# Optimization experiments

Measured on AMD Instinct MI355X. Metric: run time of the kernel, lower is better.

## Reference

```python
import jax, jax.numpy as jnp
import numpy as np
import math

N, E, C, H = 16384, 8192, 256, 8
NNZ = 262144  # incidence pairs, avg vertex degree 16


def setup_inputs() -> dict:
    key = jax.random.key(0)
    ks = jax.random.split(key, 12)
    s = 1.0 / math.sqrt(C)
    inp = {
        "X": jax.random.normal(ks[0], (N, C), dtype=jnp.float32),
        "v_ids": jax.random.randint(ks[1], (NNZ,), 0, N, dtype=jnp.int32),
        "e_ids": jax.random.randint(ks[2], (NNZ,), 0, E, dtype=jnp.int32),
        # Linear params stored as [in, out]; y = x @ W + b  (matches torch x @ W.T + b)
        "Wq": jax.random.uniform(ks[3], (C, C), jnp.float32, -s, s),
        "bq": jax.random.uniform(ks[4], (C,), jnp.float32, -s, s),
        "Wk": jax.random.uniform(ks[5], (C, C), jnp.float32, -s, s),
        "bk": jax.random.uniform(ks[6], (C,), jnp.float32, -s, s),
        "Wv": jax.random.uniform(ks[7], (C, C), jnp.float32, -s, s),
        "bv": jax.random.uniform(ks[8], (C,), jnp.float32, -s, s),
        "Wke": jax.random.uniform(ks[9], (C, C), jnp.float32, -s, s),
        "bke": jax.random.uniform(ks[10], (C,), jnp.float32, -s, s),
    }
    return inp


def reference(X, v_ids, e_ids, Wq, bq, Wk, bk, Wv, bv, Wke, bke):
    d = C // H
    scale = 1.0 / math.sqrt(d)

    Q = (X @ Wq + bq).reshape(N, H, d)
    K = (X @ Wk + bk).reshape(N, H, d)
    V = (X @ Wv + bv).reshape(N, H, d)

    # hg.v2e_aggregation(X, 'mean'): segment-mean of incident vertex features per hyperedge
    sums = jax.ops.segment_sum(X[v_ids], e_ids, num_segments=E)          # [E, C]
    cnt = jax.ops.segment_sum(jnp.ones((NNZ,), X.dtype), e_ids, num_segments=E)
    Xe = sums / jnp.maximum(cnt, 1.0)[:, None]                            # [E, C]

    Ke = Xe @ Wke + bke                                                   # [E, C]
    Qe = X @ Wq + bq                                                      # [N, C]

    # per-node attention over heads: [N, H, H]
    attn_n = jax.nn.softmax(jnp.einsum('nhd,ngd->nhg', Q, K) * scale, axis=-1)
    X_node = jnp.einsum('nhg,ngd->nhd', attn_n, V).reshape(N, C)          # [N, C]

    # node -> hyperedge attention: [N, E]
    attn_e = jax.nn.softmax((Qe @ Ke.T) * scale, axis=-1)
    X_hyperedge = attn_e @ Xe                                             # [N, C]

    out = X_node + X_hyperedge
    # is_last=False: ReLU; bn=None; dropout in eval mode (identity)
    return jax.nn.relu(out)
```

## Files before the change

### kernel.cpp

```cpp
#include <hip/hip_runtime.h>

typedef unsigned short u16;
typedef unsigned int u32;
typedef __attribute__((ext_vector_type(4))) float f32x4;
typedef __attribute__((ext_vector_type(16))) float f32x16;
typedef __attribute__((ext_vector_type(8))) short bf16x8;
typedef __attribute__((ext_vector_type(4))) short bf16x4;
typedef __attribute__((ext_vector_type(4))) u16 u16x4;

#define N_NODES 16384
#define N_EDGES 8192
#define FK_SCALE 0.17677669529663687f
#define LOG2E 1.4426950408889634f
#define C1EXP (FK_SCALE * LOG2E)

typedef const u32 __attribute__((address_space(1))) gu32;
typedef u32 __attribute__((address_space(3))) lu32;

__device__ __forceinline__ void gl_lds16(const void* g, void* l) {
  __builtin_amdgcn_global_load_lds((gu32*)g, (lu32*)l, 16, 0, 0);
}

__device__ __forceinline__ float b2f(u16 u) {
  return __builtin_bit_cast(float, (u32)u << 16);
}
__device__ __forceinline__ u16 f2b(float f) {
  u32 u = __builtin_bit_cast(u32, f);
  u += 0x7fffu + ((u >> 16) & 1u);
  return (u16)(u >> 16);
}

__global__ __launch_bounds__(256) void k_prep(const float* __restrict__ X,
                                              const int* __restrict__ e_ids,
                                              u16* __restrict__ Xb,
                                              int* __restrict__ hist,
                                              const float* __restrict__ Wq,
                                              const float* __restrict__ Wk,
                                              const float* __restrict__ Wv,
                                              const float* __restrict__ Wke,
                                              const float* __restrict__ bq,
                                              const float* __restrict__ bk,
                                              const float* __restrict__ bv,
                                              const float* __restrict__ bke,
                                              u16* __restrict__ Wt,
                                              float* __restrict__ bcat) {
  __shared__ float tile[64][65];
  int b = blockIdx.x;
  int tid = threadIdx.x;
  if (b < 4096) {
    int i = b * 256 + tid;
    f32x4 v = *(const f32x4*)(X + (size_t)i * 4);
    u16x4 r;
    r.x = f2b(v.x); r.y = f2b(v.y); r.z = f2b(v.z); r.w = f2b(v.w);
    *(u16x4*)(Xb + (size_t)i * 4) = r;
    if (tid < 64) atomicAdd(&hist[e_ids[b * 64 + tid]], 1);
    return;
  }
  int local = b - 4096;
  int w = local >> 4, rem = local & 15;
  int k0 = (rem >> 2) * 64, n0 = (rem & 3) * 64;
  const float* W = (w == 0) ? Wq : (w == 1) ? Wk : (w == 2) ? Wv : Wke;
  if (rem == 0) {
    const float* bb = (w == 0) ? bq : (w == 1) ? bk : (w == 2) ? bv : bke;
    bcat[w * 256 + tid] = bb[tid];
  }
#pragma unroll
  for (int i = 0; i < 16; i++) {
    int idx = i * 256 + tid;
    int kr = idx >> 6, nc = idx & 63;
    tile[nc][kr] = W[(k0 + kr) * 256 + n0 + nc];
  }
  __syncthreads();
#pragma unroll
  for (int i = 0; i < 16; i++) {
    int idx = i * 256 + tid;
    int nr = idx >> 6, kc = idx & 63;
    Wt[w * 65536 + (n0 + nr) * 256 + k0 + kc] = f2b(tile[nr][kc]);
  }
}

__global__ __launch_bounds__(256) void k_scan(const int* __restrict__ hist,
                                              int* __restrict__ eoff,
                                              int* __restrict__ cur) {
  __shared__ int ts[256];
  int t = threadIdx.x;
  int base = t * 32;
  int vals[32];
  int s = 0;
#pragma unroll
  for (int i = 0; i < 32; i++) { vals[i] = hist[base + i]; s += vals[i]; }
  ts[t] = s;
  __syncthreads();
  for (int off = 1; off < 256; off <<= 1) {
    int v = (t >= off) ? ts[t - off] : 0;
    __syncthreads();
    ts[t] += v;
    __syncthreads();
  }
  int ex = ts[t] - s;
#pragma unroll
  for (int i = 0; i < 32; i++) {
    eoff[base + i] = ex;
    cur[base + i] = ex;
    ex += vals[i];
  }
  if (t == 255) eoff[8192] = ex;
}

__global__ __launch_bounds__(256) void k_perm(const int* __restrict__ v_ids,
                                              const int* __restrict__ e_ids,
                                              int* __restrict__ cur,
                                              int* __restrict__ perm) {
  int base = blockIdx.x * 1024 + threadIdx.x;
#pragma unroll
  for (int k = 0; k < 4; k++) {
    int i = base + k * 256;
    int e = e_ids[i];
    int v = v_ids[i];
    int pos = atomicAdd(&cur[e], 1);
    perm[pos] = v;
  }
}

__global__ __launch_bounds__(256) void k_gather(const u16* __restrict__ Xb,
                                                const int* __restrict__ perm,
                                                const int* __restrict__ eoff,
                                                u16* __restrict__ Xe,
                                                u16* __restrict__ XeTc) {
  int tid = threadIdx.x, wave = tid >> 6, lane = tid & 63;
  int e = blockIdx.x * 4 + wave;
  int start = eoff[e], end = eoff[e + 1];
  f32x4 acc = {0.f, 0.f, 0.f, 0.f};
  for (int j = start; j < end; j++) {
    int v = perm[j];
    bf16x4 x = *(const bf16x4*)(Xb + (size_t)v * 256 + lane * 4);
#pragma unroll
    for (int c = 0; c < 4; c++) acc[c] += b2f((u16)x[c]);
  }
  float inv = 1.0f / fmaxf((float)(end - start), 1.0f);
  u16x4 r;
  r.x = f2b(acc.x * inv); r.y = f2b(acc.y * inv);
  r.z = f2b(acc.z * inv); r.w = f2b(acc.w * inv);
  *(u16x4*)(Xe + (size_t)e * 256 + lane * 4) = r;
  size_t tb = (size_t)(e >> 3) * 2048 + (e & 7);
  XeTc[tb + (lane * 4 + 0) * 8] = r.x;
  XeTc[tb + (lane * 4 + 1) * 8] = r.y;
  XeTc[tb + (lane * 4 + 2) * 8] = r.z;
  XeTc[tb + (lane * 4 + 3) * 8] = r.w;
}

__global__ __launch_bounds__(256) void k_gemm128(const u16* __restrict__ A,
                                                 const u16* __restrict__ Wt,
                                                 const float* __restrict__ bias,
                                                 u16* __restrict__ out,
                                                 int ldout, int tmode) {
  __shared__ u16 As[128 * 64];
  __shared__ u16 Bs[128 * 64];
  int tid = threadIdx.x;
  int wave = tid >> 6, lane = tid & 63;
  int quad = lane >> 4, l16 = lane & 15;
  int wm = wave >> 1, wn = wave & 1;
  int mtile = blockIdx.x * 128, ntile = blockIdx.y * 128;
  const u16* Ap = A + (size_t)mtile * 256;
  const u16* Bp = Wt + (size_t)ntile * 256;

  f32x4 acc[4][4];
#pragma unroll
  for (int am = 0; am < 4; am++)
#pragma unroll
    for (int bn = 0; bn < 4; bn++) acc[am][bn] = (f32x4){0.f, 0.f, 0.f, 0.f};

  for (int ks = 0; ks < 4; ks++) {
    __syncthreads();
#pragma unroll
    for (int i = 0; i < 4; i++) {
      int s = i * 256 + tid;
      int r = s >> 3, c = s & 7;
      gl_lds16(Ap + r * 256 + ks * 64 + ((c ^ (r & 7)) << 3), As + s * 8);
    }
#pragma unroll
    for (int i = 0; i < 4; i++) {
      int s = i * 256 + tid;
      int r = s >> 3, c = s & 7;
      gl_lds16(Bp + r * 256 + ks * 64 + ((c ^ (r & 7)) << 3), Bs + s * 8);
    }
    __syncthreads();
#pragma unroll
    for (int kc = 0; kc < 2; kc++) {
      bf16x8 a[4], b[4];
      int cc = kc * 4 + quad;
#pragma unroll
      for (int am = 0; am < 4; am++) {
        int rl = wm * 64 + am * 16 + l16;
        a[am] = *(const bf16x8*)(As + rl * 64 + ((cc ^ (rl & 7)) << 3));
      }
#pragma unroll
      for (int bn = 0; bn < 4; bn++) {
        int rl = wn * 64 + bn * 16 + l16;
        b[bn] = *(const bf16x8*)(Bs + rl * 64 + ((cc ^ (rl & 7)) << 3));
      }
#pragma unroll
      for (int am = 0; am < 4; am++)
#pragma unroll
        for (int bn = 0; bn < 4; bn++)
          acc[am][bn] = __builtin_amdgcn_mfma_f32_16x16x32_bf16(a[am], b[bn], acc[am][bn], 0, 0, 0);
    }
  }
#pragma unroll
  for (int am = 0; am < 4; am++)
#pragma unroll
    for (int bn = 0; bn < 4; bn++)
#pragma unroll
      for (int r = 0; r < 4; r++) {
        int row = mtile + wm * 64 + am * 16 + quad * 4 + r;
        int col = ntile + wn * 64 + bn * 16 + l16;
        u16 v = f2b(acc[am][bn][r] + bias[col]);
        if (tmode == 0) out[(size_t)row * ldout + col] = v;
        else out[(size_t)(col >> 3) * 65536 + row * 8 + (col & 7)] = v;
      }
}

__global__ __launch_bounds__(256, 2) void k_flash(const u16* __restrict__ QKV,
                                                  const u16* __restrict__ KebT,
                                                  const u16* __restrict__ XeTc,
                                                  u16* __restrict__ Op,
                                                  float* __restrict__ Lv) {
  extern __shared__ u16 sm[];
  u16* KeL = sm;
  u16* VLT = sm + 16384;
  u16* PL = sm + 32768;
  int tid = threadIdx.x;
  int wave = tid >> 6, lane = tid & 63;
  int l31 = lane & 31, half = lane >> 5;
  int pair = wave >> 1, kh = wave & 1;
  int qt = blockIdx.x & 255;
  int split = blockIdx.x >> 8;
  int rowp0 = qt * 64 + pair * 32;
  u16* PLp = PL + pair * 2048;

  bf16x8 qf[16];
#pragma unroll
  for (int ks = 0; ks < 16; ks++)
    qf[ks] = *(const bf16x8*)(QKV + (rowp0 + l31) * 768 + ks * 16 + half * 8);

  f32x16 o[4];
#pragma unroll
  for (int i = 0; i < 4; i++)
#pragma unroll
    for (int r = 0; r < 16; r++) o[i][r] = 0.f;
  float l[16];
#pragma unroll
  for (int r = 0; r < 16; r++) l[r] = 0.f;

  for (int ktl = 0; ktl < 64; ktl++) {
    int ktg = split * 64 + ktl;
    int kbase = ktg * 64;
    __syncthreads();
#pragma unroll
    for (int i = 0; i < 8; i++) {
      int s = i * 256 + tid;
      int c = s >> 6, r = s & 63;
      gl_lds16(KebT + ((size_t)c * 8192 + kbase + r) * 8, KeL + s * 8);
    }
    int kb8 = ktg * 8;
#pragma unroll
    for (int i = 0; i < 8; i++) {
      int s = i * 256 + tid;
      int kc = s >> 8, ch = s & 255;
      gl_lds16(XeTc + ((size_t)(kb8 + kc) * 256 + ch) * 8, VLT + s * 8);
    }
    __syncthreads();

    f32x16 sc0, sc1;
#pragma unroll
    for (int r = 0; r < 16; r++) { sc0[r] = 0.f; sc1[r] = 0.f; }
#pragma unroll
    for (int ks = 0; ks < 8; ks++) {
      int c0 = ks * 2 + half;
      int c1 = (ks + 8) * 2 + half;
      bf16x8 kb0 = *(const bf16x8*)(KeL + c0 * 512 + (kh * 32 + l31) * 8);
      bf16x8 kb1 = *(const bf16x8*)(KeL + c1 * 512 + (kh * 32 + l31) * 8);
      sc0 = __builtin_amdgcn_mfma_f32_32x32x16_bf16(qf[ks], kb0, sc0, 0, 0, 0);
      sc1 = __builtin_amdgcn_mfma_f32_32x32x16_bf16(qf[ks + 8], kb1, sc1, 0, 0, 0);
    }
#pragma unroll
    for (int reg = 0; reg < 16; reg++) {
      float pv = __builtin_amdgcn_exp2f((sc0[reg] + sc1[reg]) * C1EXP);
      l[reg] += pv;
      int row = (reg & 3) + 8 * (reg >> 2) + 4 * half;
      int col = kh * 32 + l31;
      PLp[row * 64 + (((col >> 3) ^ (row & 7)) << 3) + (col & 7)] = f2b(pv);
    }
    __syncthreads();
    bf16x8 pf[4];
#pragma unroll
    for (int ks = 0; ks < 4; ks++) {
      int pc = ks * 2 + half;
      pf[ks] = *(const bf16x8*)(PLp + l31 * 64 + ((pc ^ (l31 & 7)) << 3));
    }
#pragma unroll
    for (int ct = 0; ct < 4; ct++) {
#pragma unroll
      for (int ks = 0; ks < 4; ks++) {
        int kc = ks * 2 + half;
        int ch = kh * 128 + ct * 32 + l31;
        bf16x8 vb = *(const bf16x8*)(VLT + kc * 2048 + ch * 8);
        o[ct] = __builtin_amdgcn_mfma_f32_32x32x16_bf16(pf[ks], vb, o[ct], 0, 0, 0);
      }
    }
  }

#pragma unroll
  for (int off = 1; off < 32; off <<= 1)
#pragma unroll
    for (int r = 0; r < 16; r++) l[r] += __shfl_xor(l[r], off, 64);
  if (l31 == 0) {
#pragma unroll
    for (int reg = 0; reg < 16; reg++) {
      int row = (reg & 3) + 8 * (reg >> 2) + 4 * half;
      Lv[(split * 2 + kh) * N_NODES + rowp0 + row] = l[reg];
    }
  }

  size_t obase = (size_t)split * N_NODES * 256;
#pragma unroll
  for (int ct = 0; ct < 4; ct++)
#pragma unroll
    for (int reg = 0; reg < 16; reg++) {
      int row = rowp0 + (reg & 3) + 8 * (reg >> 2) + 4 * half;
      int col = kh * 128 + ct * 32 + l31;
      Op[obase + (size_t)row * 256 + col] = f2b(o[ct][reg]);
    }
}

__global__ __launch_bounds__(256) void k_comb(const u16* __restrict__ QKV,
                                              const u16* __restrict__ Op,
                                              const float* __restrict__ Lv,
                                              float* __restrict__ out) {
  int idx = blockIdx.x * 256 + threadIdx.x;
  int n = idx >> 6, lane = idx & 63;
  int h = lane >> 3, g = lane & 7;
  const u16* base = QKV + n * 768;
  const bf16x8* qp = (const bf16x8*)(base + h * 32);
  const bf16x8* kp = (const bf16x8*)(base + 256 + g * 32);
  float s = 0.f;
#pragma unroll
  for (int t = 0; t < 4; t++) {
    bf16x8 qv = qp[t], kv = kp[t];
#pragma unroll
    for (int j = 0; j < 8; j++) s += b2f((u16)qv[j]) * b2f((u16)kv[j]);
  }
  s *= FK_SCALE;
  float mx = s;
#pragma unroll
  for (int off = 1; off < 8; off <<= 1) mx = fmaxf(mx, __shfl_xor(mx, off, 64));
  float p = __builtin_amdgcn_exp2f((s - mx) * LOG2E);
  float lsum = p;
#pragma unroll
  for (int off = 1; off < 8; off <<= 1) lsum += __shfl_xor(lsum, off, 64);
  float attn = p / lsum;
  float a4[4] = {0.f, 0.f, 0.f, 0.f};
#pragma unroll
  for (int g2 = 0; g2 < 8; g2++) {
    float a = __shfl(attn, (lane & 56) | g2, 64);
    bf16x4 vv = *(const bf16x4*)(base + 512 + g2 * 32 + g * 4);
#pragma unroll
    for (int j = 0; j < 4; j++) a4[j] += a * b2f((u16)vv[j]);
  }
  int c4 = lane * 4;
  float L = 0.f;
#pragma unroll
  for (int sl = 0; sl < 4; sl++) L += Lv[sl * N_NODES + n];
  f32x4 acc = {0.f, 0.f, 0.f, 0.f};
#pragma unroll
  for (int sp = 0; sp < 2; sp++) {
    u16x4 ov = *(const u16x4*)(Op + (size_t)sp * N_NODES * 256 + (size_t)n * 256 + c4);
    acc.x += b2f(ov.x);
    acc.y += b2f(ov.y);
    acc.z += b2f(ov.z);
    acc.w += b2f(ov.w);
  }
  float invL = 1.0f / L;
  f32x4 res;
  res.x = fmaxf(acc.x * invL + a4[0], 0.f);
  res.y = fmaxf(acc.y * invL + a4[1], 0.f);
  res.z = fmaxf(acc.z * invL + a4[2], 0.f);
  res.w = fmaxf(acc.w * invL + a4[3], 0.f);
  *(f32x4*)(out + (size_t)n * 256 + c4) = res;
}

extern "C" void kernel_launch(void* const* d_in, const int* in_sizes, int n_in,
                              void* d_out, int out_size, void* d_ws, size_t ws_size,
                              hipStream_t stream) {
  const float* X = (const float*)d_in[0];
  const int* v_ids = (const int*)d_in[1];
  const int* e_ids = (const int*)d_in[2];
  const float* Wq = (const float*)d_in[3];
  const float* bq = (const float*)d_in[4];
  const float* Wk = (const float*)d_in[5];
  const float* bk = (const float*)d_in[6];
  const float* Wv = (const float*)d_in[7];
  const float* bv = (const float*)d_in[8];
  const float* Wke = (const float*)d_in[9];
  const float* bke = (const float*)d_in[10];
  float* out = (float*)d_out;

  char* ws = (char*)d_ws;
  u16* Xb = (u16*)(ws);
  u16* QKV = (u16*)(ws + 8388608);
  u16* Wt = (u16*)(ws + 33554432);
  float* bcat = (float*)(ws + 34078720);
  int* hist = (int*)(ws + 34082816);
  int* eoff = (int*)(ws + 34115584);
  int* cur = (int*)(ws + 34152448);
  int* perm = (int*)(ws + 34185216);
  u16* Xe = (u16*)(ws + 35233792);
  u16* XeTc = (u16*)(ws + 39428096);
  u16* KebT = (u16*)(ws + 43622400);
  u16* Op = (u16*)(ws + 64593920);
  float* Lv = (float*)(ws + 98148352);

  hipMemsetAsync(hist, 0, 32768, stream);
  k_prep<<<4160, 256, 0, stream>>>(X, e_ids, Xb, hist, Wq, Wk, Wv, Wke,
                                   bq, bk, bv, bke, Wt, bcat);
  k_scan<<<1, 256, 0, stream>>>(hist, eoff, cur);
  k_perm<<<256, 256, 0, stream>>>(v_ids, e_ids, cur, perm);
  k_gather<<<2048, 256, 0, stream>>>(Xb, perm, eoff, Xe, XeTc);
  k_gemm128<<<dim3(128, 6), 256, 0, stream>>>(Xb, Wt, bcat, QKV, 768, 0);
  k_gemm128<<<dim3(64, 2), 256, 0, stream>>>(Xe, Wt + 3 * 65536, bcat + 768, KebT, 0, 1);
  hipFuncSetAttribute((const void*)k_flash, hipFuncAttributeMaxDynamicSharedMemorySize,
                      73728);
  k_flash<<<512, 256, 73728, stream>>>(QKV, KebT, XeTc, Op, Lv);
  k_comb<<<4096, 256, 0, stream>>>(QKV, Op, Lv, out);
}
```

Measured before the change: 350.8 us.

## Overlap Ke/Xe tile loads with MFMA in flash and merge gather with QKV GEMM

In the flash kernel, the next Ke tile is now loaded into LDS while the P·V MFMAs run. The Xe value tile is loaded while the QK score MFMAs run. This removes one barrier per iteration and hides global-to-LDS latency behind compute. The hyperedge gather and the QKV projection GEMM are merged into one launch with block-index dispatch. The gather also prefetches up to 64 perm indices per wave and broadcasts them with shuffles. Correctness relies on barriers draining the outstanding LDS-direct loads before consumers read them.

```diff
diff --git a/kernel.cpp b/kernel.cpp
--- a/kernel.cpp
+++ b/kernel.cpp
@@ -122,22 +122,98 @@
   }
 }
 
-__global__ __launch_bounds__(256) void k_gather(const u16* __restrict__ Xb,
-                                                const int* __restrict__ perm,
-                                                const int* __restrict__ eoff,
-                                                u16* __restrict__ Xe,
-                                                u16* __restrict__ XeTc) {
-  int tid = threadIdx.x, wave = tid >> 6, lane = tid & 63;
-  int e = blockIdx.x * 4 + wave;
+__global__ __launch_bounds__(256) void k_gg(const u16* __restrict__ Xb,
+                                            const int* __restrict__ perm,
+                                            const int* __restrict__ eoff,
+                                            u16* __restrict__ Xe,
+                                            u16* __restrict__ XeTc,
+                                            const u16* __restrict__ Wt,
+                                            const float* __restrict__ bcat,
+                                            u16* __restrict__ QKV) {
+  __shared__ u16 As[128 * 64];
+  __shared__ u16 Bs[128 * 64];
+  int b = blockIdx.x;
+  int tid = threadIdx.x;
+  int wave = tid >> 6, lane = tid & 63;
+  if (b < 768) {
+    int quad = lane >> 4, l16 = lane & 15;
+    int wm = wave >> 1, wn = wave & 1;
+    int mtile = (b & 127) * 128, ntile = (b >> 7) * 128;
+    const u16* Ap = Xb + (size_t)mtile * 256;
+    const u16* Bp = Wt + (size_t)ntile * 256;
+    f32x4 acc[4][4];
+#pragma unroll
+    for (int am = 0; am < 4; am++)
+#pragma unroll
+      for (int bn = 0; bn < 4; bn++) acc[am][bn] = (f32x4){0.f, 0.f, 0.f, 0.f};
+    for (int ks = 0; ks < 4; ks++) {
+      __syncthreads();
+#pragma unroll
+      for (int i = 0; i < 4; i++) {
+        int s = i * 256 + tid;
+        int r = s >> 3, c = s & 7;
+        gl_lds16(Ap + r * 256 + ks * 64 + ((c ^ (r & 7)) << 3), As + s * 8);
+      }
+#pragma unroll
+      for (int i = 0; i < 4; i++) {
+        int s = i * 256 + tid;
+        int r = s >> 3, c = s & 7;
+        gl_lds16(Bp + r * 256 + ks * 64 + ((c ^ (r & 7)) << 3), Bs + s * 8);
+      }
+      __syncthreads();
+#pragma unroll
+      for (int kc = 0; kc < 2; kc++) {
+        bf16x8 a[4], bb[4];
+        int cc = kc * 4 + quad;
+#pragma unroll
+        for (int am = 0; am < 4; am++) {
+          int rl = wm * 64 + am * 16 + l16;
+          a[am] = *(const bf16x8*)(As + rl * 64 + ((cc ^ (rl & 7)) << 3));
+        }
+#pragma unroll
+        for (int bn = 0; bn < 4; bn++) {
+          int rl = wn * 64 + bn * 16 + l16;
+          bb[bn] = *(const bf16x8*)(Bs + rl * 64 + ((cc ^ (rl & 7)) << 3));
+        }
+#pragma unroll
+        for (int am = 0; am < 4; am++)
+#pragma unroll
+          for (int bn = 0; bn < 4; bn++)
+            acc[am][bn] = __builtin_amdgcn_mfma_f32_16x16x32_bf16(a[am], bb[bn], acc[am][bn], 0, 0, 0);
+      }
+    }
+#pragma unroll
+    for (int am = 0; am < 4; am++)
+#pragma unroll
+      for (int bn = 0; bn < 4; bn++)
+#pragma unroll
+        for (int r = 0; r < 4; r++) {
+          int row = mtile + wm * 64 + am * 16 + quad * 4 + r;
+          int col = ntile + wn * 64 + bn * 16 + l16;
+          QKV[(size_t)row * 768 + col] = f2b(acc[am][bn][r] + bcat[col]);
+        }
+    return;
+  }
+  int e = (b - 768) * 4 + wave;
   int start = eoff[e], end = eoff[e + 1];
+  int cnt = end - start;
+  int pidx = 0;
+  if (lane < cnt) pidx = perm[start + lane];
   f32x4 acc = {0.f, 0.f, 0.f, 0.f};
-  for (int j = start; j < end; j++) {
+  int n1 = cnt < 64 ? cnt : 64;
+  for (int j = 0; j < n1; j++) {
+    int v = __shfl(pidx, j, 64);
+    bf16x4 x = *(const bf16x4*)(Xb + (size_t)v * 256 + lane * 4);
+#pragma unroll
+    for (int c = 0; c < 4; c++) acc[c] += b2f((u16)x[c]);
+  }
+  for (int j = start + 64; j < end; j++) {
     int v = perm[j];
     bf16x4 x = *(const bf16x4*)(Xb + (size_t)v * 256 + lane * 4);
 #pragma unroll
     for (int c = 0; c < 4; c++) acc[c] += b2f((u16)x[c]);
   }
-  float inv = 1.0f / fmaxf((float)(end - start), 1.0f);
+  float inv = 1.0f / fmaxf((float)cnt, 1.0f);
   u16x4 r;
   r.x = f2b(acc.x * inv); r.y = f2b(acc.y * inv);
   r.z = f2b(acc.z * inv); r.w = f2b(acc.w * inv);
@@ -149,11 +225,10 @@
   XeTc[tb + (lane * 4 + 3) * 8] = r.w;
 }
 
-__global__ __launch_bounds__(256) void k_gemm128(const u16* __restrict__ A,
-                                                 const u16* __restrict__ Wt,
-                                                 const float* __restrict__ bias,
-                                                 u16* __restrict__ out,
-                                                 int ldout, int tmode) {
+__global__ __launch_bounds__(256) void k_gemmke(const u16* __restrict__ A,
+                                                const u16* __restrict__ Wt,
+                                                const float* __restrict__ bias,
+                                                u16* __restrict__ KebT) {
   __shared__ u16 As[128 * 64];
   __shared__ u16 Bs[128 * 64];
   int tid = threadIdx.x;
@@ -163,13 +238,11 @@
   int mtile = blockIdx.x * 128, ntile = blockIdx.y * 128;
   const u16* Ap = A + (size_t)mtile * 256;
   const u16* Bp = Wt + (size_t)ntile * 256;
-
   f32x4 acc[4][4];
 #pragma unroll
   for (int am = 0; am < 4; am++)
 #pragma unroll
     for (int bn = 0; bn < 4; bn++) acc[am][bn] = (f32x4){0.f, 0.f, 0.f, 0.f};
-
   for (int ks = 0; ks < 4; ks++) {
     __syncthreads();
 #pragma unroll
@@ -214,10 +287,28 @@
       for (int r = 0; r < 4; r++) {
         int row = mtile + wm * 64 + am * 16 + quad * 4 + r;
         int col = ntile + wn * 64 + bn * 16 + l16;
-        u16 v = f2b(acc[am][bn][r] + bias[col]);
-        if (tmode == 0) out[(size_t)row * ldout + col] = v;
-        else out[(size_t)(col >> 3) * 65536 + row * 8 + (col & 7)] = v;
-      }
+        KebT[(size_t)(col >> 3) * 65536 + row * 8 + (col & 7)] = f2b(acc[am][bn][r] + bias[col]);
+      }
+}
+
+__device__ __forceinline__ void stage_k(const u16* __restrict__ KebT, u16* KeL,
+                                        int kbase, int tid) {
+#pragma unroll
+  for (int i = 0; i < 8; i++) {
+    int s = i * 256 + tid;
+    int c = s >> 6, r = s & 63;
+    gl_lds16(KebT + ((size_t)c * 8192 + kbase + r) * 8, KeL + s * 8);
+  }
+}
+__device__ __forceinline__ void stage_v(const u16* __restrict__ XeTc, u16* VLT,
+                                        int ktg, int tid) {
+  int kb8 = ktg * 8;
+#pragma unroll
+  for (int i = 0; i < 8; i++) {
+    int s = i * 256 + tid;
+    int kc = s >> 8, ch = s & 255;
+    gl_lds16(XeTc + ((size_t)(kb8 + kc) * 256 + ch) * 8, VLT + s * 8);
+  }
 }
 
 __global__ __launch_bounds__(256, 2) void k_flash(const u16* __restrict__ QKV,
@@ -252,24 +343,12 @@
 #pragma unroll
   for (int r = 0; r < 16; r++) l[r] = 0.f;
 
+  stage_k(KebT, KeL, (split * 64) * 64, tid);
+
   for (int ktl = 0; ktl < 64; ktl++) {
     int ktg = split * 64 + ktl;
-    int kbase = ktg * 64;
     __syncthreads();
-#pragma unroll
-    for (int i = 0; i < 8; i++) {
-      int s = i * 256 + tid;
-      int c = s >> 6, r = s & 63;
-      gl_lds16(KebT + ((size_t)c * 8192 + kbase + r) * 8, KeL + s * 8);
-    }
-    int kb8 = ktg * 8;
-#pragma unroll
-    for (int i = 0; i < 8; i++) {
-      int s = i * 256 + tid;
-      int kc = s >> 8, ch = s & 255;
-      gl_lds16(XeTc + ((size_t)(kb8 + kc) * 256 + ch) * 8, VLT + s * 8);
-    }
-    __syncthreads();
+    stage_v(XeTc, VLT, ktg, tid);
 
     f32x16 sc0, sc1;
 #pragma unroll
@@ -292,6 +371,8 @@
       PLp[row * 64 + (((col >> 3) ^ (row & 7)) << 3) + (col & 7)] = f2b(pv);
     }
     __syncthreads();
+    if (ktl + 1 < 64) stage_k(KebT, KeL, (ktg + 1) * 64, tid);
+
     bf16x8 pf[4];
 #pragma unroll
     for (int ks = 0; ks < 4; ks++) {
@@ -425,9 +506,8 @@
                                    bq, bk, bv, bke, Wt, bcat);
   k_scan<<<1, 256, 0, stream>>>(hist, eoff, cur);
   k_perm<<<256, 256, 0, stream>>>(v_ids, e_ids, cur, perm);
-  k_gather<<<2048, 256, 0, stream>>>(Xb, perm, eoff, Xe, XeTc);
-  k_gemm128<<<dim3(128, 6), 256, 0, stream>>>(Xb, Wt, bcat, QKV, 768, 0);
-  k_gemm128<<<dim3(64, 2), 256, 0, stream>>>(Xe, Wt + 3 * 65536, bcat + 768, KebT, 0, 1);
+  k_gg<<<2816, 256, 0, stream>>>(Xb, perm, eoff, Xe, XeTc, Wt, bcat, QKV);
+  k_gemmke<<<dim3(64, 2), 256, 0, stream>>>(Xe, Wt + 3 * 65536, bcat + 768, KebT);
   hipFuncSetAttribute((const void*)k_flash, hipFuncAttributeMaxDynamicSharedMemorySize,
                       73728);
   k_flash<<<512, 256, 73728, stream>>>(QKV, KebT, XeTc, Op, Lv);
```

After: 342.1 us. 1.03x faster.
